# Kernel optimization log

Measured on AMD Instinct MI355X. Metric: run time of the kernel, lower is better.

The kernel has to match this reference:

```python
import jax, jax.numpy as jnp
import numpy as np

N_NODES = 100000
N_EDGES = 1600000
D = 128


def _sage_conv(x, src, dst, W_l, b_l, W_r, num_nodes):
    # gather source-node features along edges, mean-aggregate at destination
    msg_sum = jax.ops.segment_sum(x[src], dst, num_segments=num_nodes)  # [N, D]
    cnt = jax.ops.segment_sum(jnp.ones((src.shape[0], 1), x.dtype), dst,
                              num_segments=num_nodes)                   # [N, 1]
    agg = msg_sum / jnp.maximum(cnt, 1.0)
    # PyG SAGEConv: lin_l(aggregated) + bias + lin_r(self), root linear has no bias
    return agg @ W_l + b_l + x @ W_r


def setup_inputs() -> dict:
    key = jax.random.key(0)
    ks = jax.random.split(key, 8)
    scale = 1.0 / np.sqrt(D)
    x = jax.random.normal(ks[0], (N_NODES, D), dtype=jnp.float32)
    edge_index = jax.random.randint(ks[1], (2, N_EDGES), 0, N_NODES, dtype=jnp.int64)
    W_l1 = jax.random.normal(ks[2], (D, D), dtype=jnp.float32) * scale
    b_l1 = jnp.zeros((D,), dtype=jnp.float32)
    W_r1 = jax.random.normal(ks[3], (D, D), dtype=jnp.float32) * scale
    W_l2 = jax.random.normal(ks[4], (D, D), dtype=jnp.float32) * scale
    b_l2 = jnp.zeros((D,), dtype=jnp.float32)
    W_r2 = jax.random.normal(ks[5], (D, D), dtype=jnp.float32) * scale
    return {"x": x, "edge_index": edge_index, "W_l1": W_l1, "b_l1": b_l1,
            "W_r1": W_r1, "W_l2": W_l2, "b_l2": b_l2, "W_r2": W_r2}


def reference(x, edge_index, W_l1, b_l1, W_r1, W_l2, b_l2, W_r2):
    src, dst = edge_index[0], edge_index[1]
    n = x.shape[0]
    h = jax.nn.relu(_sage_conv(x, src, dst, W_l1, b_l1, W_r1, n))
    out = _sage_conv(h, src, dst, W_l2, b_l2, W_r2, n)
    return out
```

## Files before the change

### kernel.cpp

```cpp
#include <hip/hip_runtime.h>
#include <hip/hip_bf16.h>

#define DF 128
#define BSH 7
#define BNODES (1 << BSH)
#define SRCBITS 17
#define SRCMASK ((1u << SRCBITS) - 1u)
#define NBLK 512
#define SLABSH 13
#define NKEYS (BNODES * 16)
#define EBCAP 2560
#define CURSTR 16

typedef __attribute__((ext_vector_type(8))) short short8;
typedef __attribute__((ext_vector_type(4))) float floatx4;

__device__ __forceinline__ unsigned short f2bf(float f) {
  unsigned u = __float_as_uint(f);
  u += 0x7fffu + ((u >> 16) & 1u);
  return (unsigned short)(u >> 16);
}
__device__ __forceinline__ float bflo(unsigned u) { return __uint_as_float(u << 16); }
__device__ __forceinline__ float bfhi(unsigned u) { return __uint_as_float(u & 0xffff0000u); }


__global__ __launch_bounds__(256) void prep(const float* __restrict__ x,
                                            unsigned short* __restrict__ xb, int n4, int cb,
                                            const float* __restrict__ W0,
                                            const float* __restrict__ W1,
                                            const float* __restrict__ W2,
                                            const float* __restrict__ W3,
                                            unsigned short* __restrict__ wf,
                                            int* __restrict__ cur, int nb) {
  int bid = blockIdx.x, t = threadIdx.x;
  if (bid < cb) {
    int i = bid * 256 + t;
    if (i < n4) {
      float4 v = ((const float4*)x)[i];
      union { unsigned short u[4]; uint2 d; } o;
      o.u[0] = f2bf(v.x); o.u[1] = f2bf(v.y); o.u[2] = f2bf(v.z); o.u[3] = f2bf(v.w);
      ((uint2*)xb)[i] = o.d;
    }
  } else if (bid < cb + 256) {
    int bb = bid - cb;
    int m = bb >> 6;
    const float* W = (m == 0) ? W0 : (m == 1) ? W1 : (m == 2) ? W2 : W3;
    int tt = (bb & 63) * 256 + t;
    int j = tt & 7, lane = (tt >> 3) & 63, ktnt = tt >> 9;
    int nt = ktnt & 7, kt = ktnt >> 3;
    int k = kt * 32 + (lane >> 4) * 8 + j;
    int ncol = nt * 16 + (lane & 15);
    wf[m * 16384 + tt] = f2bf(W[k * DF + ncol]);
  } else {
    for (int b = t; b < nb; b += 256) cur[b * CURSTR] = b * EBCAP;
  }
}

__global__ __launch_bounds__(256) void scatter2(const int* __restrict__ src,
                                                const int* __restrict__ dst,
                                                int* __restrict__ cur,
                                                unsigned* __restrict__ ebuf,
                                                int e, int nb, int chunk) {
  __shared__ int cnt[1024];
  __shared__ int runb[1024];
  int t = threadIdx.x, blk = blockIdx.x;
  for (int b = t; b < nb; b += 256) cnt[b] = 0;
  __syncthreads();
  int s = blk * chunk, en = min(e, s + chunk);
  int sv[13], dv[13];
  int cntl = 0;
#pragma unroll
  for (int j = 0; j < 13; ++j) {
    int i = s + t + j * 256;
    if (i < en) { sv[j] = src[i]; dv[j] = dst[i]; cntl = j + 1; }
  }
#pragma unroll
  for (int j = 0; j < 13; ++j)
    if (j < cntl) atomicAdd(&cnt[dv[j] >> BSH], 1);
  __syncthreads();
  for (int b = t; b < nb; b += 256) {
    int c = cnt[b];
    runb[b] = (c > 0) ? atomicAdd(&cur[b * CURSTR], c) : 0;
  }
  __syncthreads();
#pragma unroll
  for (int j = 0; j < 13; ++j)
    if (j < cntl) {
      int d = dv[j];
      int p = atomicAdd(&runb[d >> BSH], 1);
      ebuf[p] = ((unsigned)(d & (BNODES - 1)) << SRCBITS) | (unsigned)sv[j];
    }
}

__global__ __launch_bounds__(256) void fill_fine(const unsigned* __restrict__ ebuf,
                                                 const int* __restrict__ cend,
                                                 int* __restrict__ rs,
                                                 int* __restrict__ csr, int n) {
  __shared__ int hist[NKEYS];
  __shared__ int cur[NKEYS];
  __shared__ int wsum[4];
  int b = blockIdx.x;
  int t = threadIdx.x;
  for (int i = t; i < NKEYS; i += 256) hist[i] = 0;
  __syncthreads();
  int s = b * EBCAP, e = cend[b * CURSTR];
  for (int i = s + t; i < e; i += 256) {
    unsigned p = ebuf[i];
    int key = (int)((p >> SRCBITS) << 4) | (int)((p & SRCMASK) >> SLABSH);
    atomicAdd(&hist[key], 1);
  }
  __syncthreads();
  int v[8], sum = 0;
#pragma unroll
  for (int j = 0; j < 8; ++j) { v[j] = hist[t * 8 + j]; sum += v[j]; }
  int lane = t & 63, wid = t >> 6;
  int S = sum;
#pragma unroll
  for (int o = 1; o < 64; o <<= 1) {
    int u = __shfl_up(S, o);
    if (lane >= o) S += u;
  }
  if (lane == 63) wsum[wid] = S;
  __syncthreads();
  if (wid == 0 && lane < 4) {
    int ws = wsum[lane];
#pragma unroll
    for (int o = 1; o < 4; o <<= 1) {
      int u = __shfl_up(ws, o);
      if (lane >= o) ws += u;
    }
    wsum[lane] = ws;
  }
  __syncthreads();
  int base = (S - sum) + ((wid > 0) ? wsum[wid - 1] : 0);
#pragma unroll
  for (int j = 0; j < 8; ++j) { cur[t * 8 + j] = base; base += v[j]; }
  __syncthreads();
  if (t < BNODES) {
    int g = (b << BSH) + t;
    if (g < n) {
      int endoff = (t == BNODES - 1) ? (e - s) : cur[(t + 1) << 4];
      rs[g] = s + endoff;
    }
  }
  __syncthreads();
  for (int i = s + t; i < e; i += 256) {
    unsigned p = ebuf[i];
    int key = (int)((p >> SRCBITS) << 4) | (int)((p & SRCMASK) >> SLABSH);
    int r = atomicAdd(&cur[key], 1);
    csr[s + r] = (int)(p & SRCMASK);
  }
}

__global__ __launch_bounds__(256) void agg_pull(const uint4* __restrict__ feat,
                                                const int* __restrict__ rs,
                                                const int* __restrict__ csr,
                                                uint4* __restrict__ out, int n) {
  int node = (blockIdx.x * 256 + threadIdx.x) >> 4;
  int l = threadIdx.x & 15;
  if (node >= n) return;
  int lr = node & (BNODES - 1);
  int s = lr ? rs[node - 1] : (node >> BSH) * EBCAP;
  int e = rs[node];
  float a0 = 0.f, a1 = 0.f, a2 = 0.f, a3 = 0.f;
  float a4 = 0.f, a5 = 0.f, a6 = 0.f, a7 = 0.f;
  int i = s;
  for (; i + 7 < e; i += 8) {
    int idx[8];
#pragma unroll
    for (int k = 0; k < 8; ++k) idx[k] = csr[i + k];
    uint4 u[8];
#pragma unroll
    for (int k = 0; k < 8; ++k) u[k] = feat[idx[k] * 16 + l];
#pragma unroll
    for (int k = 0; k < 8; ++k) {
      a0 += bflo(u[k].x); a1 += bfhi(u[k].x);
      a2 += bflo(u[k].y); a3 += bfhi(u[k].y);
      a4 += bflo(u[k].z); a5 += bfhi(u[k].z);
      a6 += bflo(u[k].w); a7 += bfhi(u[k].w);
    }
  }
  for (; i < e; ++i) {
    uint4 u = feat[csr[i] * 16 + l];
    a0 += bflo(u.x); a1 += bfhi(u.x);
    a2 += bflo(u.y); a3 += bfhi(u.y);
    a4 += bflo(u.z); a5 += bfhi(u.z);
    a6 += bflo(u.w); a7 += bfhi(u.w);
  }
  float sc = 1.0f / (float)max(e - s, 1);
  uint4 o;
  o.x = (unsigned)f2bf(a0 * sc) | ((unsigned)f2bf(a1 * sc) << 16);
  o.y = (unsigned)f2bf(a2 * sc) | ((unsigned)f2bf(a3 * sc) << 16);
  o.z = (unsigned)f2bf(a4 * sc) | ((unsigned)f2bf(a5 * sc) << 16);
  o.w = (unsigned)f2bf(a6 * sc) | ((unsigned)f2bf(a7 * sc) << 16);
  out[node * 16 + l] = o;
}

__global__ __launch_bounds__(256) void gemm_sage(const unsigned short* __restrict__ Aagg,
                                                 const unsigned short* __restrict__ Aself,
                                                 const unsigned short* __restrict__ WFl,
                                                 const unsigned short* __restrict__ WFr,
                                                 const float* __restrict__ bias,
                                                 void* __restrict__ outp, int n,
                                                 int relu_out_bf16) {
  __shared__ unsigned short Wsl[DF * DF];
  __shared__ unsigned short Wsr[DF * DF];
  int t = threadIdx.x;
  {
    const uint4* wl4 = (const uint4*)WFl;
    const uint4* wr4 = (const uint4*)WFr;
    uint4* sl4 = (uint4*)Wsl;
    uint4* sr4 = (uint4*)Wsr;
#pragma unroll
    for (int i = 0; i < 8; ++i) {
      sl4[i * 256 + t] = wl4[i * 256 + t];
      sr4[i * 256 + t] = wr4[i * 256 + t];
    }
  }
  __syncthreads();

  int wave = t >> 6;
  int lane = t & 63;
  int l16 = lane & 15, quad = lane >> 4;
  int rbase = (blockIdx.x * 4 + wave) * 32;
  if (rbase >= n) return;

  floatx4 acc[2][8];
#pragma unroll
  for (int a = 0; a < 2; ++a)
#pragma unroll
    for (int b = 0; b < 8; ++b) acc[a][b] = (floatx4)0.0f;

  int r0 = min(rbase + l16, n - 1);
  int r1 = min(rbase + 16 + l16, n - 1);

#pragma unroll
  for (int s = 0; s < 2; ++s) {
    const unsigned short* A = s ? Aself : Aagg;
    const unsigned short* W = s ? Wsr : Wsl;
    short8 a0[4], a1[4];
#pragma unroll
    for (int kt = 0; kt < 4; ++kt) {
      a0[kt] = *(const short8*)(A + r0 * DF + kt * 32 + quad * 8);
      a1[kt] = *(const short8*)(A + r1 * DF + kt * 32 + quad * 8);
    }
#pragma unroll
    for (int kt = 0; kt < 4; ++kt) {
#pragma unroll
      for (int nt = 0; nt < 8; ++nt) {
        short8 bf = *(const short8*)(W + (((kt * 8 + nt) * 64) + lane) * 8);
        acc[0][nt] = __builtin_amdgcn_mfma_f32_16x16x32_bf16(a0[kt], bf, acc[0][nt], 0, 0, 0);
        acc[1][nt] = __builtin_amdgcn_mfma_f32_16x16x32_bf16(a1[kt], bf, acc[1][nt], 0, 0, 0);
      }
    }
  }

  float bv[8];
#pragma unroll
  for (int nt = 0; nt < 8; ++nt) bv[nt] = bias[nt * 16 + l16];

  if (relu_out_bf16) {
    unsigned short* O = (unsigned short*)outp;
#pragma unroll
    for (int rb = 0; rb < 2; ++rb)
#pragma unroll
      for (int i = 0; i < 4; ++i) {
        int row = rbase + rb * 16 + quad * 4 + i;
        if (row < n) {
#pragma unroll
          for (int nt = 0; nt < 8; ++nt) {
            float v = acc[rb][nt][i] + bv[nt];
            O[row * DF + nt * 16 + l16] = f2bf(fmaxf(v, 0.0f));
          }
        }
      }
  } else {
    float* O = (float*)outp;
#pragma unroll
    for (int rb = 0; rb < 2; ++rb)
#pragma unroll
      for (int i = 0; i < 4; ++i) {
        int row = rbase + rb * 16 + quad * 4 + i;
        if (row < n) {
#pragma unroll
          for (int nt = 0; nt < 8; ++nt)
            O[row * DF + nt * 16 + l16] = acc[rb][nt][i] + bv[nt];
        }
      }
  }
}


extern "C" void kernel_launch(void* const* d_in, const int* in_sizes, int n_in,
                              void* d_out, int out_size, void* d_ws, size_t ws_size,
                              hipStream_t stream) {
  const float* x   = (const float*)d_in[0];
  const int*   ei  = (const int*)d_in[1];
  const float* Wl1 = (const float*)d_in[2];
  const float* bl1 = (const float*)d_in[3];
  const float* Wr1 = (const float*)d_in[4];
  const float* Wl2 = (const float*)d_in[5];
  const float* bl2 = (const float*)d_in[6];
  const float* Wr2 = (const float*)d_in[7];

  int n = in_sizes[0] / DF;
  int e = in_sizes[1] / 2;
  const int* srcv = ei;
  const int* dstv = ei + e;
  int nb = (n + BNODES - 1) >> BSH;
  int chunk = (e + NBLK - 1) / NBLK;

  char* ws = (char*)d_ws;
  size_t off = 0;
  auto alloc = [&](size_t bytes) {
    void* p = ws + off;
    off = (off + bytes + 255) & ~(size_t)255;
    return p;
  };
  int* cur   = (int*)alloc((size_t)nb * CURSTR * 4);
  int* rs    = (int*)alloc((size_t)n * 4);
  unsigned* ebuf = (unsigned*)alloc((size_t)nb * EBCAP * 4);
  int* csr   = (int*)alloc((size_t)nb * EBCAP * 4);
  unsigned short* xb   = (unsigned short*)alloc((size_t)n * DF * 2);
  unsigned short* hb   = (unsigned short*)alloc((size_t)n * DF * 2);
  unsigned short* aggb = (unsigned short*)alloc((size_t)n * DF * 2);
  unsigned short* wf   = (unsigned short*)alloc(4 * DF * DF * 2);
  unsigned short* wfl1 = wf;
  unsigned short* wfr1 = wf + 16384;
  unsigned short* wfl2 = wf + 32768;
  unsigned short* wfr2 = wf + 49152;

  int n4 = n * DF / 4;
  int cb = (n4 + 255) / 256;
  prep<<<cb + 256 + 1, 256, 0, stream>>>(x, xb, n4, cb, Wl1, Wr1, Wl2, Wr2, wf, cur, nb);
  scatter2<<<NBLK, 256, 0, stream>>>(srcv, dstv, cur, ebuf, e, nb, chunk);
  fill_fine<<<nb, 256, 0, stream>>>(ebuf, cur, rs, csr, n);

  agg_pull<<<(n * 16 + 255) / 256, 256, 0, stream>>>((const uint4*)xb, rs, csr,
                                                     (uint4*)aggb, n);
  gemm_sage<<<(n + 127) / 128, 256, 0, stream>>>(aggb, xb, wfl1, wfr1, bl1, hb, n, 1);
  agg_pull<<<(n * 16 + 255) / 256, 256, 0, stream>>>((const uint4*)hb, rs, csr,
                                                     (uint4*)aggb, n);
  gemm_sage<<<(n + 127) / 128, 256, 0, stream>>>(aggb, hb, wfl2, wfr2, bl2, d_out, n, 0);
}
```

Measured before the change: 323.8 us.

## Fuse edge scatter into prep kernel and use full wavefront per node in aggregation

Merges the edge-bucketing scatter with the x/weight bf16 conversion into one kernel launch. The bucket cursors are now zeroed by a memset and hold relative offsets, which fill_fine adds to the bucket base. The aggregation kernel now gives each node a 64-lane wavefront, with four 16-lane groups each pulling a different neighbor, then combines them with cross-lane shuffles. This aims to cut launch overhead and raise memory-level parallelism for short neighbor lists, at the cost of idle lanes on padded iterations and an extra memset call.

```diff
diff --git a/kernel.cpp b/kernel.cpp
--- a/kernel.cpp
+++ b/kernel.cpp
@@ -24,25 +24,50 @@
 __device__ __forceinline__ float bfhi(unsigned u) { return __uint_as_float(u & 0xffff0000u); }
 
 
-__global__ __launch_bounds__(256) void prep(const float* __restrict__ x,
-                                            unsigned short* __restrict__ xb, int n4, int cb,
-                                            const float* __restrict__ W0,
-                                            const float* __restrict__ W1,
-                                            const float* __restrict__ W2,
-                                            const float* __restrict__ W3,
-                                            unsigned short* __restrict__ wf,
-                                            int* __restrict__ cur, int nb) {
+__global__ __launch_bounds__(256) void fused_prep(const int* __restrict__ src,
+                                                  const int* __restrict__ dst,
+                                                  int* __restrict__ cur,
+                                                  unsigned* __restrict__ ebuf,
+                                                  int e, int nb, int chunk,
+                                                  const float* __restrict__ x,
+                                                  unsigned short* __restrict__ xb, int n4,
+                                                  const float* __restrict__ W0,
+                                                  const float* __restrict__ W1,
+                                                  const float* __restrict__ W2,
+                                                  const float* __restrict__ W3,
+                                                  unsigned short* __restrict__ wf) {
   int bid = blockIdx.x, t = threadIdx.x;
-  if (bid < cb) {
-    int i = bid * 256 + t;
-    if (i < n4) {
-      float4 v = ((const float4*)x)[i];
-      union { unsigned short u[4]; uint2 d; } o;
-      o.u[0] = f2bf(v.x); o.u[1] = f2bf(v.y); o.u[2] = f2bf(v.z); o.u[3] = f2bf(v.w);
-      ((uint2*)xb)[i] = o.d;
-    }
-  } else if (bid < cb + 256) {
-    int bb = bid - cb;
+  if (bid < NBLK) {
+    __shared__ int cnt[1024];
+    __shared__ int runb[1024];
+    for (int b = t; b < nb; b += 256) cnt[b] = 0;
+    __syncthreads();
+    int s = bid * chunk, en = min(e, s + chunk);
+    int sv[13], dv[13];
+    int cntl = 0;
+#pragma unroll
+    for (int j = 0; j < 13; ++j) {
+      int i = s + t + j * 256;
+      if (i < en) { sv[j] = src[i]; dv[j] = dst[i]; cntl = j + 1; }
+    }
+#pragma unroll
+    for (int j = 0; j < 13; ++j)
+      if (j < cntl) atomicAdd(&cnt[dv[j] >> BSH], 1);
+    __syncthreads();
+    for (int b = t; b < nb; b += 256) {
+      int c = cnt[b];
+      runb[b] = (c > 0) ? (b * EBCAP + atomicAdd(&cur[b * CURSTR], c)) : 0;
+    }
+    __syncthreads();
+#pragma unroll
+    for (int j = 0; j < 13; ++j)
+      if (j < cntl) {
+        int d = dv[j];
+        int p = atomicAdd(&runb[d >> BSH], 1);
+        ebuf[p] = ((unsigned)(d & (BNODES - 1)) << SRCBITS) | (unsigned)sv[j];
+      }
+  } else if (bid < NBLK + 256) {
+    int bb = bid - NBLK;
     int m = bb >> 6;
     const float* W = (m == 0) ? W0 : (m == 1) ? W1 : (m == 2) ? W2 : W3;
     int tt = (bb & 63) * 256 + t;
@@ -52,44 +77,14 @@
     int ncol = nt * 16 + (lane & 15);
     wf[m * 16384 + tt] = f2bf(W[k * DF + ncol]);
   } else {
-    for (int b = t; b < nb; b += 256) cur[b * CURSTR] = b * EBCAP;
-  }
-}
-
-__global__ __launch_bounds__(256) void scatter2(const int* __restrict__ src,
-                                                const int* __restrict__ dst,
-                                                int* __restrict__ cur,
-                                                unsigned* __restrict__ ebuf,
-                                                int e, int nb, int chunk) {
-  __shared__ int cnt[1024];
-  __shared__ int runb[1024];
-  int t = threadIdx.x, blk = blockIdx.x;
-  for (int b = t; b < nb; b += 256) cnt[b] = 0;
-  __syncthreads();
-  int s = blk * chunk, en = min(e, s + chunk);
-  int sv[13], dv[13];
-  int cntl = 0;
-#pragma unroll
-  for (int j = 0; j < 13; ++j) {
-    int i = s + t + j * 256;
-    if (i < en) { sv[j] = src[i]; dv[j] = dst[i]; cntl = j + 1; }
-  }
-#pragma unroll
-  for (int j = 0; j < 13; ++j)
-    if (j < cntl) atomicAdd(&cnt[dv[j] >> BSH], 1);
-  __syncthreads();
-  for (int b = t; b < nb; b += 256) {
-    int c = cnt[b];
-    runb[b] = (c > 0) ? atomicAdd(&cur[b * CURSTR], c) : 0;
-  }
-  __syncthreads();
-#pragma unroll
-  for (int j = 0; j < 13; ++j)
-    if (j < cntl) {
-      int d = dv[j];
-      int p = atomicAdd(&runb[d >> BSH], 1);
-      ebuf[p] = ((unsigned)(d & (BNODES - 1)) << SRCBITS) | (unsigned)sv[j];
-    }
+    int i = (bid - NBLK - 256) * 256 + t;
+    if (i < n4) {
+      float4 v = ((const float4*)x)[i];
+      union { unsigned short u[4]; uint2 d; } o;
+      o.u[0] = f2bf(v.x); o.u[1] = f2bf(v.y); o.u[2] = f2bf(v.z); o.u[3] = f2bf(v.w);
+      ((uint2*)xb)[i] = o.d;
+    }
+  }
 }
 
 __global__ __launch_bounds__(256) void fill_fine(const unsigned* __restrict__ ebuf,
@@ -103,7 +98,7 @@
   int t = threadIdx.x;
   for (int i = t; i < NKEYS; i += 256) hist[i] = 0;
   __syncthreads();
-  int s = b * EBCAP, e = cend[b * CURSTR];
+  int s = b * EBCAP, e = s + cend[b * CURSTR];
   for (int i = s + t; i < e; i += 256) {
     unsigned p = ebuf[i];
     int key = (int)((p >> SRCBITS) << 4) | (int)((p & SRCMASK) >> SLABSH);
@@ -156,44 +151,55 @@
                                                 const int* __restrict__ rs,
                                                 const int* __restrict__ csr,
                                                 uint4* __restrict__ out, int n) {
-  int node = (blockIdx.x * 256 + threadIdx.x) >> 4;
-  int l = threadIdx.x & 15;
+  int node = (blockIdx.x * 256 + threadIdx.x) >> 6;
   if (node >= n) return;
-  int lr = node & (BNODES - 1);
-  int s = lr ? rs[node - 1] : (node >> BSH) * EBCAP;
+  int lane = threadIdx.x & 63;
+  int g = lane >> 4, l = lane & 15;
+  int s = (node & (BNODES - 1)) ? rs[node - 1] : (node >> BSH) * EBCAP;
   int e = rs[node];
   float a0 = 0.f, a1 = 0.f, a2 = 0.f, a3 = 0.f;
   float a4 = 0.f, a5 = 0.f, a6 = 0.f, a7 = 0.f;
-  int i = s;
-  for (; i + 7 < e; i += 8) {
-    int idx[8];
-#pragma unroll
-    for (int k = 0; k < 8; ++k) idx[k] = csr[i + k];
-    uint4 u[8];
-#pragma unroll
-    for (int k = 0; k < 8; ++k) u[k] = feat[idx[k] * 16 + l];
-#pragma unroll
-    for (int k = 0; k < 8; ++k) {
-      a0 += bflo(u[k].x); a1 += bfhi(u[k].x);
-      a2 += bflo(u[k].y); a3 += bfhi(u[k].y);
-      a4 += bflo(u[k].z); a5 += bfhi(u[k].z);
-      a6 += bflo(u[k].w); a7 += bfhi(u[k].w);
-    }
-  }
-  for (; i < e; ++i) {
-    uint4 u = feat[csr[i] * 16 + l];
-    a0 += bflo(u.x); a1 += bfhi(u.x);
-    a2 += bflo(u.y); a3 += bfhi(u.y);
-    a4 += bflo(u.z); a5 += bfhi(u.z);
-    a6 += bflo(u.w); a7 += bfhi(u.w);
-  }
-  float sc = 1.0f / (float)max(e - s, 1);
-  uint4 o;
-  o.x = (unsigned)f2bf(a0 * sc) | ((unsigned)f2bf(a1 * sc) << 16);
-  o.y = (unsigned)f2bf(a2 * sc) | ((unsigned)f2bf(a3 * sc) << 16);
-  o.z = (unsigned)f2bf(a4 * sc) | ((unsigned)f2bf(a5 * sc) << 16);
-  o.w = (unsigned)f2bf(a6 * sc) | ((unsigned)f2bf(a7 * sc) << 16);
-  out[node * 16 + l] = o;
+  int em1 = e - 1;
+  for (int i = s; i < e; i += 16) {
+    int i0 = i + g, i1 = i + g + 4, i2 = i + g + 8, i3 = i + g + 12;
+    int c0 = csr[min(i0, em1)];
+    int c1 = csr[min(i1, em1)];
+    int c2 = csr[min(i2, em1)];
+    int c3 = csr[min(i3, em1)];
+    uint4 u0 = feat[c0 * 16 + l];
+    uint4 u1 = feat[c1 * 16 + l];
+    uint4 u2 = feat[c2 * 16 + l];
+    uint4 u3 = feat[c3 * 16 + l];
+    if (i0 >= e) { u0.x = 0u; u0.y = 0u; u0.z = 0u; u0.w = 0u; }
+    if (i1 >= e) { u1.x = 0u; u1.y = 0u; u1.z = 0u; u1.w = 0u; }
+    if (i2 >= e) { u2.x = 0u; u2.y = 0u; u2.z = 0u; u2.w = 0u; }
+    if (i3 >= e) { u3.x = 0u; u3.y = 0u; u3.z = 0u; u3.w = 0u; }
+    a0 += bflo(u0.x); a1 += bfhi(u0.x); a2 += bflo(u0.y); a3 += bfhi(u0.y);
+    a4 += bflo(u0.z); a5 += bfhi(u0.z); a6 += bflo(u0.w); a7 += bfhi(u0.w);
+    a0 += bflo(u1.x); a1 += bfhi(u1.x); a2 += bflo(u1.y); a3 += bfhi(u1.y);
+    a4 += bflo(u1.z); a5 += bfhi(u1.z); a6 += bflo(u1.w); a7 += bfhi(u1.w);
+    a0 += bflo(u2.x); a1 += bfhi(u2.x); a2 += bflo(u2.y); a3 += bfhi(u2.y);
+    a4 += bflo(u2.z); a5 += bfhi(u2.z); a6 += bflo(u2.w); a7 += bfhi(u2.w);
+    a0 += bflo(u3.x); a1 += bfhi(u3.x); a2 += bflo(u3.y); a3 += bfhi(u3.y);
+    a4 += bflo(u3.z); a5 += bfhi(u3.z); a6 += bflo(u3.w); a7 += bfhi(u3.w);
+  }
+  a0 += __shfl_xor(a0, 16); a0 += __shfl_xor(a0, 32);
+  a1 += __shfl_xor(a1, 16); a1 += __shfl_xor(a1, 32);
+  a2 += __shfl_xor(a2, 16); a2 += __shfl_xor(a2, 32);
+  a3 += __shfl_xor(a3, 16); a3 += __shfl_xor(a3, 32);
+  a4 += __shfl_xor(a4, 16); a4 += __shfl_xor(a4, 32);
+  a5 += __shfl_xor(a5, 16); a5 += __shfl_xor(a5, 32);
+  a6 += __shfl_xor(a6, 16); a6 += __shfl_xor(a6, 32);
+  a7 += __shfl_xor(a7, 16); a7 += __shfl_xor(a7, 32);
+  if (g == 0) {
+    float sc = 1.0f / (float)max(e - s, 1);
+    uint4 o;
+    o.x = (unsigned)f2bf(a0 * sc) | ((unsigned)f2bf(a1 * sc) << 16);
+    o.y = (unsigned)f2bf(a2 * sc) | ((unsigned)f2bf(a3 * sc) << 16);
+    o.z = (unsigned)f2bf(a4 * sc) | ((unsigned)f2bf(a5 * sc) << 16);
+    o.w = (unsigned)f2bf(a6 * sc) | ((unsigned)f2bf(a7 * sc) << 16);
+    out[node * 16 + l] = o;
+  }
 }
 
 __global__ __launch_bounds__(256) void gemm_sage(const unsigned short* __restrict__ Aagg,
@@ -332,14 +338,15 @@
 
   int n4 = n * DF / 4;
   int cb = (n4 + 255) / 256;
-  prep<<<cb + 256 + 1, 256, 0, stream>>>(x, xb, n4, cb, Wl1, Wr1, Wl2, Wr2, wf, cur, nb);
-  scatter2<<<NBLK, 256, 0, stream>>>(srcv, dstv, cur, ebuf, e, nb, chunk);
+  hipMemsetAsync(cur, 0, (size_t)nb * CURSTR * 4, stream);
+  fused_prep<<<NBLK + 256 + cb, 256, 0, stream>>>(srcv, dstv, cur, ebuf, e, nb, chunk,
+                                                  x, xb, n4, Wl1, Wr1, Wl2, Wr2, wf);
   fill_fine<<<nb, 256, 0, stream>>>(ebuf, cur, rs, csr, n);
 
-  agg_pull<<<(n * 16 + 255) / 256, 256, 0, stream>>>((const uint4*)xb, rs, csr,
+  agg_pull<<<(n * 64 + 255) / 256, 256, 0, stream>>>((const uint4*)xb, rs, csr,
                                                      (uint4*)aggb, n);
   gemm_sage<<<(n + 127) / 128, 256, 0, stream>>>(aggb, xb, wfl1, wfr1, bl1, hb, n, 1);
-  agg_pull<<<(n * 16 + 255) / 256, 256, 0, stream>>>((const uint4*)hb, rs, csr,
+  agg_pull<<<(n * 64 + 255) / 256, 256, 0, stream>>>((const uint4*)hb, rs, csr,
                                                      (uint4*)aggb, n);
   gemm_sage<<<(n + 127) / 128, 256, 0, stream>>>(aggb, hb, wfl2, wfr2, bl2, d_out, n, 0);
 }
```

Result: faster. 308.8 us (-4.6%).
